# Optimization experiments

Hardware: AMD Instinct MI355X
Metric: run time of the kernel (lower is better)

## Reference

```python
import jax, jax.numpy as jnp
import numpy as np

B, T, D, H, DK = 4, 1024, 512, 8, 64
L = 2 * T - 1  # relative position length
EPS = 1e-3     # keras LayerNormalization default epsilon


def rel_shift(x, klen):
    # x: [B, H, T, L] with L = 2T-1 -> [B, H, T, klen] (Transformer-XL shift)
    b, h, t, l = x.shape
    x = x.reshape(b, h, l, t)[:, :, 1:, :]
    x = x.reshape(b, h, t, l - 1)
    return x[:, :, :, :klen]


def setup_inputs() -> dict:
    key = jax.random.key(0)
    ks = jax.random.split(key, 16)
    s = 0.02
    return {
        "x": jax.random.normal(ks[0], (B, T, D), jnp.float32),
        "pos": jax.random.normal(ks[1], (B, L, D), jnp.float32),
        "content_bias": jax.random.normal(ks[2], (H, DK), jnp.float32) * s,
        "pos_bias": jax.random.normal(ks[3], (H, DK), jnp.float32) * s,
        "gamma": jnp.ones((D,), jnp.float32),
        "beta": jnp.zeros((D,), jnp.float32),
        "Wq": jax.random.normal(ks[4], (D, H, DK), jnp.float32) * s,
        "bq": jnp.zeros((H, DK), jnp.float32),
        "Wk": jax.random.normal(ks[5], (D, H, DK), jnp.float32) * s,
        "bk": jnp.zeros((H, DK), jnp.float32),
        "Wv": jax.random.normal(ks[6], (D, H, DK), jnp.float32) * s,
        "bv": jnp.zeros((H, DK), jnp.float32),
        "Wp": jax.random.normal(ks[7], (D, H, DK), jnp.float32) * s,
        "Wo": jax.random.normal(ks[8], (H, DK, D), jnp.float32) * s,
        "bo": jnp.zeros((D,), jnp.float32),
    }


def reference(x, pos, content_bias, pos_bias, gamma, beta,
              Wq, bq, Wk, bk, Wv, bv, Wp, Wo, bo):
    # pre-norm LayerNorm
    mean = jnp.mean(x, axis=-1, keepdims=True)
    var = jnp.var(x, axis=-1, keepdims=True)
    y = (x - mean) * jax.lax.rsqrt(var + EPS) * gamma + beta

    # per-head projections
    q = jnp.einsum("bid,dhk->bihk", y, Wq) + bq      # [B,T,H,DK]
    k = jnp.einsum("bjd,dhk->bjhk", y, Wk) + bk
    v = jnp.einsum("bjd,dhk->bjhk", y, Wv) + bv
    p = jnp.einsum("bld,dhk->blhk", pos, Wp)          # [B,L,H,DK], no bias

    # Transformer-XL content + positional scores
    content = jnp.einsum("bihk,bjhk->bhij", q + content_bias, k)   # [B,H,T,T]
    positional = jnp.einsum("bihk,blhk->bhil", q + pos_bias, p)    # [B,H,T,L]
    positional = rel_shift(positional, content.shape[-1])          # [B,H,T,T]

    scores = (content + positional) / np.sqrt(DK).astype(np.float32)
    attn = jax.nn.softmax(scores, axis=-1)

    o = jnp.einsum("bhij,bjhk->bihk", attn, v)       # [B,T,H,DK]
    out = jnp.einsum("bihk,hkd->bid", o, Wo) + bo    # [B,T,D]

    # dropout is identity at inference; residual with factor=1.0
    return x + out
```

## Files before the change

kernel.cpp:

```cpp
#include <hip/hip_runtime.h>
#include <hip/hip_bf16.h>

typedef __hip_bfloat16 bf16;
typedef __attribute__((ext_vector_type(8))) short short8;
typedef __attribute__((ext_vector_type(4))) float f32x4;

#define B_  4
#define T_  1024
#define D_  512
#define H_  8
#define DK_ 64
#define L_  2047

__device__ __forceinline__ float b2f(bf16 v) { return __bfloat162float(v); }
__device__ __forceinline__ bf16  f2b(float v) { return __float2bfloat16(v); }
__device__ __forceinline__ float bits2f(unsigned short u) {
    return __uint_as_float(((unsigned int)u) << 16);
}
__device__ __forceinline__ unsigned short fbits(float v) {
    bf16 h = f2b(v); return *(unsigned short*)&h;
}

#define MFMA16(a, b, c) __builtin_amdgcn_mfma_f32_16x16x32_bf16(a, b, c, 0, 0, 0)
#define GLD_LDS16(g, l) __builtin_amdgcn_global_load_lds( \
    (const __attribute__((address_space(1))) unsigned int*)(g), \
    (__attribute__((address_space(3))) unsigned int*)(l), 16, 0, 0)

__global__ __launch_bounds__(256) void prep_all(
        const float* __restrict__ Wq, const float* __restrict__ Wk,
        const float* __restrict__ Wv, const float* __restrict__ Wp,
        const float* __restrict__ Wo,
        const float* __restrict__ bq, const float* __restrict__ bk,
        const float* __restrict__ bv,
        const float* __restrict__ pos, const float* __restrict__ x,
        const float* __restrict__ gamma, const float* __restrict__ beta,
        bf16* __restrict__ Wqkv_t, bf16* __restrict__ Wp_t, bf16* __restrict__ Wo_t,
        float* __restrict__ biasq, bf16* __restrict__ pos_bf, bf16* __restrict__ y) {
    __shared__ float tl[32][33];
    __shared__ float ws1[4], ws2[4];
    const int blk = blockIdx.x;
    const int t = threadIdx.x;

    if (blk < 1280) {
        const int z = blk >> 8, rem = blk & 255;
        const float* W; bf16* Wt; int roff;
        switch (z) {
            case 0: W = Wq; Wt = Wqkv_t; roff = 0;    break;
            case 1: W = Wk; Wt = Wqkv_t; roff = 512;  break;
            case 2: W = Wv; Wt = Wqkv_t; roff = 1024; break;
            case 3: W = Wp; Wt = Wp_t;   roff = 0;    break;
            default: W = Wo; Wt = Wo_t;  roff = 0;    break;
        }
        const int n0 = (rem & 15) * 32, k0 = (rem >> 4) * 32;
        const int tx = t & 31, ty = t >> 5;
#pragma unroll
        for (int r = 0; r < 4; ++r)
            tl[ty + r * 8][tx] = W[(size_t)(k0 + ty + r * 8) * 512 + n0 + tx];
        __syncthreads();
#pragma unroll
        for (int r = 0; r < 4; ++r)
            Wt[(size_t)(roff + n0 + ty + r * 8) * 512 + k0 + tx] = f2b(tl[tx][ty + r * 8]);
    } else if (blk < 1286) {
        int i = (blk - 1280) * 256 + t;
        biasq[i] = (i < 512) ? bq[i] : (i < 1024) ? bk[i - 512] : bv[i - 1024];
    } else if (blk < 3333) {
        size_t i = ((size_t)(blk - 1286) * 256 + t) * 8;
        float4 a = *(const float4*)(pos + i);
        float4 c = *(const float4*)(pos + i + 4);
        uint4 wv;
        wv.x = ((unsigned)fbits(a.y) << 16) | fbits(a.x);
        wv.y = ((unsigned)fbits(a.w) << 16) | fbits(a.z);
        wv.z = ((unsigned)fbits(c.y) << 16) | fbits(c.x);
        wv.w = ((unsigned)fbits(c.w) << 16) | fbits(c.z);
        *(uint4*)((unsigned short*)pos_bf + i) = wv;
    } else {
        const int row = blk - 3333;
        const float* xr = x + (size_t)row * D_;
        float v0 = xr[t];
        float v1 = xr[t + 256];
        float s  = v0 + v1;
        float s2 = v0 * v0 + v1 * v1;
#pragma unroll
        for (int off = 32; off > 0; off >>= 1) {
            s  += __shfl_down(s,  off, 64);
            s2 += __shfl_down(s2, off, 64);
        }
        const int wid = t >> 6, lane = t & 63;
        if (!lane) { ws1[wid] = s; ws2[wid] = s2; }
        __syncthreads();
        float S  = ws1[0] + ws1[1] + ws1[2] + ws1[3];
        float S2 = ws2[0] + ws2[1] + ws2[2] + ws2[3];
        float mean = S * (1.f / D_);
        float var  = S2 * (1.f / D_) - mean * mean;
        float r = rsqrtf(var + 1e-3f);
        bf16* yr = y + (size_t)row * D_;
        yr[t]       = f2b((v0 - mean) * r * gamma[t]       + beta[t]);
        yr[t + 256] = f2b((v1 - mean) * r * gamma[t + 256] + beta[t + 256]);
    }
}

template <bool C_F32>
__device__ __forceinline__ void gemm_body(
        const bf16* __restrict__ A, const bf16* __restrict__ Wt,
        const float* __restrict__ bias, const float* __restrict__ resid,
        void* __restrict__ Cv, int M, size_t seg_elems, int m0, int n0,
        unsigned short (*A_s)[32], unsigned short (*B_s)[32]) {
    const int t = threadIdx.x;
    const int w = t >> 6, lane = t & 63;
    const int quad = lane >> 4, n16 = lane & 15;
    const int wm = (w >> 1) * 64, wn = (w & 1) * 64;

    f32x4 acc[4][4];
#pragma unroll
    for (int a = 0; a < 4; ++a)
#pragma unroll
        for (int b = 0; b < 4; ++b) acc[a][b] = (f32x4){0.f, 0.f, 0.f, 0.f};

    const int ar = lane >> 2, ac8 = (lane & 3) * 8;
    auto stage = [&](int k0, int buf) {
        const int bo = buf << 7;
#pragma unroll
        for (int ps = 0; ps < 2; ++ps) {
            int br = (ps * 4 + w) * 16;
            GLD_LDS16(A  + (size_t)(m0 + br + ar) * 512 + k0 + ac8, &A_s[bo + br][0]);
            GLD_LDS16(Wt + (size_t)(n0 + br + ar) * 512 + k0 + ac8, &B_s[bo + br][0]);
        }
    };
    stage(0, 0);
    int cur = 0;
    for (int k0 = 0; k0 < 512; k0 += 32) {
        __syncthreads();
        if (k0 + 32 < 512) stage(k0 + 32, cur ^ 1);
        const int bo = cur << 7;
        short8 af[4], bfr[4];
#pragma unroll
        for (int i = 0; i < 4; ++i) {
            af[i]  = *(const short8*)&A_s[bo + wm + i * 16 + n16][quad * 8];
            bfr[i] = *(const short8*)&B_s[bo + wn + i * 16 + n16][quad * 8];
        }
#pragma unroll
        for (int mi = 0; mi < 4; ++mi)
#pragma unroll
            for (int ni = 0; ni < 4; ++ni)
                acc[mi][ni] = MFMA16(af[mi], bfr[ni], acc[mi][ni]);
        cur ^= 1;
    }

    const int seg = n0 >> 9;
#pragma unroll
    for (int mi = 0; mi < 4; ++mi) {
#pragma unroll
        for (int r = 0; r < 4; ++r) {
            int row = m0 + wm + mi * 16 + quad * 4 + r;
            if (row >= M) continue;
#pragma unroll
            for (int ni = 0; ni < 4; ++ni) {
                int col  = n0 + wn + ni * 16 + n16;
                int coll = col & 511;
                float vv = acc[mi][ni][r];
                if (bias) vv += bias[col];
                if constexpr (C_F32) {
                    float* C = (float*)Cv + seg * seg_elems;
                    if (resid) vv += resid[(size_t)row * 512 + coll];
                    C[(size_t)row * 512 + coll] = vv;
                } else {
                    bf16* C = (bf16*)Cv + seg * seg_elems;
                    C[(size_t)row * 512 + coll] = f2b(vv);
                }
            }
        }
    }
}

__global__ __launch_bounds__(256) void gemm_qkvp(
        const bf16* __restrict__ y, const bf16* __restrict__ pos_bf,
        const bf16* __restrict__ Wqkv_t, const bf16* __restrict__ Wp_t,
        const float* __restrict__ biasq,
        bf16* __restrict__ q, bf16* __restrict__ p, size_t seg_elems) {
    __shared__ __align__(16) unsigned short A_s[256][32];
    __shared__ __align__(16) unsigned short B_s[256][32];
    const int gid = blockIdx.x;
    if (gid < 384) {
        const int xcd = gid & 7, s = gid >> 3;
        const int n = s % 12;
        const int m = xcd * 4 + s / 12;
        gemm_body<false>(y, Wqkv_t, biasq, nullptr, q, 4096, seg_elems,
                         m * 128, n * 128, A_s, B_s);
    } else {
        const int g2 = gid - 384;
        const int xcd = g2 & 7, s = g2 >> 3;
        const int n = s & 3;
        const int m = xcd * 8 + (s >> 2);
        gemm_body<false>(pos_bf, Wp_t, nullptr, nullptr, p, 8188, 0,
                         m * 128, n * 128, A_s, B_s);
    }
}

__global__ __launch_bounds__(256) void gemm_out(
        const bf16* __restrict__ o, const bf16* __restrict__ Wo_t,
        const float* __restrict__ bo, const float* __restrict__ x,
        float* __restrict__ out) {
    __shared__ __align__(16) unsigned short A_s[256][32];
    __shared__ __align__(16) unsigned short B_s[256][32];
    const int xcd = blockIdx.x & 7, s = blockIdx.x >> 3;
    const int n = s & 3;
    const int m = xcd * 4 + (s >> 2);
    gemm_body<true>(o, Wo_t, bo, x, out, 4096, 0, m * 128, n * 128, A_s, B_s);
}

__global__ __launch_bounds__(256) void attn_mfma_kernel(
        const bf16* __restrict__ q, const bf16* __restrict__ k,
        const bf16* __restrict__ v, const bf16* __restrict__ p,
        const float* __restrict__ cbias, const float* __restrict__ pbias,
        bf16* __restrict__ o) {
    __shared__ __align__(16) unsigned short k_s[2][4096];
    __shared__ __align__(16) unsigned short pw_s[2][8192];
    __shared__ __align__(16) unsigned short vt_s[2][64][72];
    __shared__ __align__(16) unsigned short gbuf[4][16][72];
    __shared__ float cb_s[64], pb_s[64];
    __shared__ float wrap_s;

    const int fid  = blockIdx.x;
    const int xcd  = fid & 7;
    const int slot = fid >> 3;
    const int i0   = (slot & 15) * 64;
    const int g    = (slot >> 4) * 8 + xcd;
    const int h    = g & 7;
    const int b    = g >> 3;

    const int t  = threadIdx.x;
    const int w    = t >> 6;
    const int lane = t & 63;
    const int quad = lane >> 4;
    const int n16  = lane & 15;
    const int h64  = h * 64;
    const float sc_scale = 0.125f * 1.4426950408889634f;

    if (t < 64)       cb_s[t]      = cbias[h64 + t];
    else if (t < 128) pb_s[t - 64] = pbias[h64 + t - 64];

    const int l8 = lane >> 3, l7 = lane & 7;
    const int clog8 = (l7 ^ l8) * 8;
    const unsigned short* ksrc[2];
    const unsigned short* psrc[4];
#pragma unroll
    for (int ps = 0; ps < 2; ++ps) {
        int row = (w * 2 + ps) * 8 + l8;
        ksrc[ps] = (const unsigned short*)k + ((size_t)(b * T_ + row) * 512 + h64 + clog8);
    }
    const int slb = T_ - i0 - 63;
#pragma unroll
    for (int ps = 0; ps < 4; ++ps) {
        int row = (w * 4 + ps) * 8 + l8;
        psrc[ps] = (const unsigned short*)p + ((size_t)(b * L_ + slb + row) * 512 + h64 + clog8);
    }
    auto stage = [&](int j0n, int nxt) {
        size_t joff = (size_t)j0n * 512;
#pragma unroll
        for (int ps = 0; ps < 2; ++ps)
            GLD_LDS16(ksrc[ps] + joff, &k_s[nxt][(w * 2 + ps) * 512]);
#pragma unroll
        for (int ps = 0; ps < 4; ++ps)
            GLD_LDS16(psrc[ps] + joff, &pw_s[nxt][(w * 4 + ps) * 512]);
    };

    const int vd2 = (t & 31) * 2, vjg = t >> 5;
    const unsigned short* vsrc = (const unsigned short*)v +
        ((size_t)(b * T_ + vjg * 8) * 512 + h64 + vd2);
    unsigned int vReg[8];
    auto vload = [&](int j0n) {
        const unsigned short* vg = vsrc + (size_t)j0n * 512;
#pragma unroll
        for (int e = 0; e < 8; ++e) vReg[e] = *(const unsigned int*)(vg + (size_t)e * 512);
    };
    auto vwrite = [&](int nxt) {
        uint4 wlo, whi;
        wlo.x = (vReg[0] & 0xffffu) | (vReg[1] << 16);
        wlo.y = (vReg[2] & 0xffffu) | (vReg[3] << 16);
        wlo.z = (vReg[4] & 0xffffu) | (vReg[5] << 16);
        wlo.w = (vReg[6] & 0xffffu) | (vReg[7] << 16);
        whi.x = (vReg[0] >> 16) | (vReg[1] & 0xffff0000u);
        whi.y = (vReg[2] >> 16) | (vReg[3] & 0xffff0000u);
        whi.z = (vReg[4] >> 16) | (vReg[5] & 0xffff0000u);
        whi.w = (vReg[6] >> 16) | (vReg[7] & 0xffff0000u);
        *(uint4*)&vt_s[nxt][vd2][vjg * 8]     = wlo;
        *(uint4*)&vt_s[nxt][vd2 + 1][vjg * 8] = whi;
    };

    stage(0, 0);
    vload(0);
    __syncthreads();

    short8 ac[2], ap[2];
    {
        const unsigned short* qrow = (const unsigned short*)q +
            ((size_t)(b * T_ + i0 + 16 * w + n16) * 512 + h64);
#pragma unroll
        for (int kc = 0; kc < 2; ++kc) {
            uint4 u = *(const uint4*)(qrow + kc * 32 + quad * 8);
            const unsigned short* uv = (const unsigned short*)&u;
            unsigned short* acp = (unsigned short*)&ac[kc];
            unsigned short* app = (unsigned short*)&ap[kc];
#pragma unroll
            for (int e = 0; e < 8; ++e) {
                int d = kc * 32 + quad * 8 + e;
                float qv = bits2f(uv[e]);
                acp[e] = fbits((qv + cb_s[d]) * sc_scale);
                app[e] = fbits((qv + pb_s[d]) * sc_scale);
            }
        }
    }
    if (i0 == 0 && t < 64) {
        float part = (b2f(q[(size_t)(b * T_ + 1) * 512 + h64 + t]) + pb_s[t]) *
                     b2f(p[(size_t)(b * L_) * 512 + h64 + t]);
#pragma unroll
        for (int m = 1; m < 64; m <<= 1) part += __shfl_xor(part, m, 64);
        if (t == 0) wrap_s = part * sc_scale;
    }
    vwrite(0);

    int srcl[4]; bool hi[4];
#pragma unroll
    for (int r = 0; r < 4; ++r) {
        int ii = quad * 4 + r;
        srcl[r] = (lane & 48) | ((n16 - ii - 1) & 15);
        hi[r]   = n16 > ii;
    }
    short8 onesb;
    {
        const short ov = (n16 == 0) ? (short)0x3F80 : (short)0;
#pragma unroll
        for (int e = 0; e < 8; ++e) onesb[e] = ov;
    }

    const int pwoff = 48 - 16 * w;
    const int swzA  = (quad ^ (n16 & 7)) * 16;
    const int swzB  = swzA ^ 64;

    f32x4 O[4], O4;
#pragma unroll
    for (int nt = 0; nt < 4; ++nt) O[nt] = (f32x4){0.f, 0.f, 0.f, 0.f};
    O4 = (f32x4){0.f, 0.f, 0.f, 0.f};

    int cur = 0;
    for (int j0 = 0; j0 < T_; j0 += 64) {
        __syncthreads();
        const int nxt = cur ^ 1;
        const bool pre = (j0 + 64 < T_);
        if (pre) { vload(j0 + 64); stage(j0 + 64, nxt); }

        const char* krA  = (const char*)&k_s[cur][0]  + n16 * 128 + swzA;
        const char* krB  = krA + (swzB - swzA);
        const char* pwrA = (const char*)&pw_s[cur][0] + (pwoff + n16) * 128 + swzA;
        const char* pwrB = pwrA + (swzB - swzA);

        f32x4 Sc[4], G[5];
#pragma unroll
        for (int nt = 0; nt < 4; ++nt) Sc[nt] = (f32x4){0.f, 0.f, 0.f, 0.f};
#pragma unroll
        for (int ct = 0; ct < 5; ++ct) G[ct] = (f32x4){0.f, 0.f, 0.f, 0.f};
        __builtin_amdgcn_s_setprio(1);
#pragma unroll
        for (int kc = 0; kc < 2; ++kc) {
#pragma unroll
            for (int nt = 0; nt < 4; ++nt) {
                short8 bk = *(const short8*)((kc ? krB : krA) + nt * 2048);
                Sc[nt] = MFMA16(ac[kc], bk, Sc[nt]);
            }
#pragma unroll
            for (int ct = 0; ct < 5; ++ct) {
                short8 bp = *(const short8*)((kc ? pwrB : pwrA) + ct * 2048);
                G[ct] = MFMA16(ap[kc], bp, G[ct]);
            }
        }
        __builtin_amdgcn_s_setprio(0);

        float pe[4][4];
#pragma unroll
        for (int r = 0; r < 4; ++r) {
            float s0 = __shfl(G[0][r], srcl[r], 64);
            float s1 = __shfl(G[1][r], srcl[r], 64);
            float s2 = __shfl(G[2][r], srcl[r], 64);
            float s3 = __shfl(G[3][r], srcl[r], 64);
            float s4 = __shfl(G[4][r], srcl[r], 64);
            pe[0][r] = Sc[0][r] + (hi[r] ? s1 : s0);
            pe[1][r] = Sc[1][r] + (hi[r] ? s2 : s1);
            pe[2][r] = Sc[2][r] + (hi[r] ? s3 : s2);
            pe[3][r] = Sc[3][r] + (hi[r] ? s4 : s3);
        }
        if (i0 == 0 && w == 0 && j0 == 960 && lane == 15)
            pe[3][0] = Sc[3][0] + wrap_s;
#pragma unroll
        for (int ct = 0; ct < 4; ++ct)
#pragma unroll
            for (int r = 0; r < 4; ++r)
                *(bf16*)&gbuf[w][quad * 4 + r][ct * 16 + n16] = f2b(exp2f(pe[ct][r]));

        __builtin_amdgcn_s_setprio(1);
#pragma unroll
        for (int kc = 0; kc < 2; ++kc) {
            short8 pa = *(const short8*)&gbuf[w][n16][kc * 32 + quad * 8];
#pragma unroll
            for (int nt = 0; nt < 4; ++nt) {
                short8 vb = *(const short8*)&vt_s[cur][nt * 16 + n16][kc * 32 + quad * 8];
                O[nt] = MFMA16(pa, vb, O[nt]);
            }
            O4 = MFMA16(pa, onesb, O4);
        }
        __builtin_amdgcn_s_setprio(0);

        if (pre) vwrite(nxt);
        cur = nxt;
    }

#pragma unroll
    for (int r = 0; r < 4; ++r) {
        float l = __shfl(O4[r], lane & 48, 64);
        float inv = 1.f / l;
        int row = i0 + 16 * w + quad * 4 + r;
#pragma unroll
        for (int nt = 0; nt < 4; ++nt)
            o[(size_t)(b * T_ + row) * 512 + h64 + nt * 16 + n16] = f2b(O[nt][r] * inv);
    }
}

extern "C" void kernel_launch(void* const* d_in, const int* in_sizes, int n_in,
                              void* d_out, int out_size, void* d_ws, size_t ws_size,
                              hipStream_t stream) {
    (void)in_sizes; (void)n_in; (void)out_size;
    const float* x     = (const float*)d_in[0];
    const float* pos   = (const float*)d_in[1];
    const float* cb    = (const float*)d_in[2];
    const float* pb    = (const float*)d_in[3];
    const float* gamma = (const float*)d_in[4];
    const float* beta  = (const float*)d_in[5];
    const float* Wq    = (const float*)d_in[6];
    const float* bq    = (const float*)d_in[7];
    const float* Wk    = (const float*)d_in[8];
    const float* bk    = (const float*)d_in[9];
    const float* Wv    = (const float*)d_in[10];
    const float* bv    = (const float*)d_in[11];
    const float* Wp    = (const float*)d_in[12];
    const float* Wo    = (const float*)d_in[13];
    const float* bo    = (const float*)d_in[14];
    float* out = (float*)d_out;

    const int BT = B_ * T_;

    const size_t sz_bt = (size_t)BT * D_;
    const size_t sz_bl = (size_t)(B_ * L_) * D_;
    const size_t sz_w  = 512 * 512;
    const size_t need  = (5 * sz_bt + sz_bl + 5 * sz_w) * sizeof(bf16) + 1536 * sizeof(float);
    if (ws_size < need) return;

    bf16* y       = (bf16*)d_ws;
    bf16* o       = y + sz_bt;
    bf16* q       = y + 2 * sz_bt;
    bf16* k       = y + 3 * sz_bt;
    bf16* v       = y + 4 * sz_bt;
    bf16* p       = y + 5 * sz_bt;
    bf16* Wqkv_t  = p + sz_bl;
    bf16* Wp_t    = Wqkv_t + 3 * sz_w;
    bf16* Wo_t    = Wp_t + sz_w;
    float* biasq  = (float*)(Wo_t + sz_w);
    bf16* pos_bf  = (bf16*)d_out;

    prep_all<<<7429, 256, 0, stream>>>(Wq, Wk, Wv, Wp, Wo, bq, bk, bv, pos, x,
                                       gamma, beta, Wqkv_t, Wp_t, Wo_t, biasq, pos_bf, y);

    gemm_qkvp<<<640, 256, 0, stream>>>(y, pos_bf, Wqkv_t, Wp_t, biasq, q, p, sz_bt);

    attn_mfma_kernel<<<512, 256, 0, stream>>>(q, k, v, p, cb, pb, o);

    gemm_out<<<128, 256, 0, stream>>>(o, Wo_t, bo, x, out);
}
```

Before: 209.1 us.

## Software-pipeline attention loop: overlap next tile QK with current softmax-PV

```diff
diff --git a/kernel.cpp b/kernel.cpp
--- a/kernel.cpp
+++ b/kernel.cpp
@@ -208,7 +208,7 @@
     gemm_body<true>(o, Wo_t, bo, x, out, 4096, 0, m * 128, n * 128, A_s, B_s);
 }
 
-__global__ __launch_bounds__(256) void attn_mfma_kernel(
+__global__ __launch_bounds__(256, 2) void attn_mfma_kernel(
         const bf16* __restrict__ q, const bf16* __restrict__ k,
         const bf16* __restrict__ v, const bf16* __restrict__ p,
         const float* __restrict__ cbias, const float* __restrict__ pbias,
@@ -220,14 +220,9 @@
     __shared__ float cb_s[64], pb_s[64];
     __shared__ float wrap_s;
 
-    const int fid  = blockIdx.x;
-    const int xcd  = fid & 7;
-    const int slot = fid >> 3;
-    const int i0   = (slot & 15) * 64;
-    const int g    = (slot >> 4) * 8 + xcd;
-    const int h    = g & 7;
-    const int b    = g >> 3;
-
+    const int i0 = blockIdx.x * 64;
+    const int h  = blockIdx.y;
+    const int b  = blockIdx.z;
     const int t  = threadIdx.x;
     const int w    = t >> 6;
     const int lane = t & 63;
@@ -317,14 +312,13 @@
         for (int m = 1; m < 64; m <<= 1) part += __shfl_xor(part, m, 64);
         if (t == 0) wrap_s = part * sc_scale;
     }
-    vwrite(0);
-
-    int srcl[4]; bool hi[4];
+
+    int srcl[4]; bool hi_[4];
 #pragma unroll
     for (int r = 0; r < 4; ++r) {
         int ii = quad * 4 + r;
         srcl[r] = (lane & 48) | ((n16 - ii - 1) & 15);
-        hi[r]   = n16 > ii;
+        hi_[r]  = n16 > ii;
     }
     short8 onesb;
     {
@@ -342,24 +336,15 @@
     for (int nt = 0; nt < 4; ++nt) O[nt] = (f32x4){0.f, 0.f, 0.f, 0.f};
     O4 = (f32x4){0.f, 0.f, 0.f, 0.f};
 
-    int cur = 0;
-    for (int j0 = 0; j0 < T_; j0 += 64) {
-        __syncthreads();
-        const int nxt = cur ^ 1;
-        const bool pre = (j0 + 64 < T_);
-        if (pre) { vload(j0 + 64); stage(j0 + 64, nxt); }
-
-        const char* krA  = (const char*)&k_s[cur][0]  + n16 * 128 + swzA;
-        const char* krB  = krA + (swzB - swzA);
-        const char* pwrA = (const char*)&pw_s[cur][0] + (pwoff + n16) * 128 + swzA;
-        const char* pwrB = pwrA + (swzB - swzA);
-
-        f32x4 Sc[4], G[5];
+    auto qk = [&](f32x4 (&Sc)[4], f32x4 (&G)[5], int buf) {
+        const char* krA  = (const char*)&k_s[buf][0]  + n16 * 128 + swzA;
+        const char* krB  = (const char*)&k_s[buf][0]  + n16 * 128 + swzB;
+        const char* pwrA = (const char*)&pw_s[buf][0] + (pwoff + n16) * 128 + swzA;
+        const char* pwrB = (const char*)&pw_s[buf][0] + (pwoff + n16) * 128 + swzB;
 #pragma unroll
         for (int nt = 0; nt < 4; ++nt) Sc[nt] = (f32x4){0.f, 0.f, 0.f, 0.f};
 #pragma unroll
         for (int ct = 0; ct < 5; ++ct) G[ct] = (f32x4){0.f, 0.f, 0.f, 0.f};
-        __builtin_amdgcn_s_setprio(1);
 #pragma unroll
         for (int kc = 0; kc < 2; ++kc) {
 #pragma unroll
@@ -373,8 +358,9 @@
                 G[ct] = MFMA16(ap[kc], bp, G[ct]);
             }
         }
-        __builtin_amdgcn_s_setprio(0);
-
+    };
+
+    auto sm_pv = [&](const f32x4 (&Sc)[4], const f32x4 (&G)[5], int vb, bool dowrap) {
         float pe[4][4];
 #pragma unroll
         for (int r = 0; r < 4; ++r) {
@@ -383,35 +369,55 @@
             float s2 = __shfl(G[2][r], srcl[r], 64);
             float s3 = __shfl(G[3][r], srcl[r], 64);
             float s4 = __shfl(G[4][r], srcl[r], 64);
-            pe[0][r] = Sc[0][r] + (hi[r] ? s1 : s0);
-            pe[1][r] = Sc[1][r] + (hi[r] ? s2 : s1);
-            pe[2][r] = Sc[2][r] + (hi[r] ? s3 : s2);
-            pe[3][r] = Sc[3][r] + (hi[r] ? s4 : s3);
-        }
-        if (i0 == 0 && w == 0 && j0 == 960 && lane == 15)
+            pe[0][r] = Sc[0][r] + (hi_[r] ? s1 : s0);
+            pe[1][r] = Sc[1][r] + (hi_[r] ? s2 : s1);
+            pe[2][r] = Sc[2][r] + (hi_[r] ? s3 : s2);
+            pe[3][r] = Sc[3][r] + (hi_[r] ? s4 : s3);
+        }
+        if (dowrap && i0 == 0 && w == 0 && lane == 15)
             pe[3][0] = Sc[3][0] + wrap_s;
 #pragma unroll
         for (int ct = 0; ct < 4; ++ct)
 #pragma unroll
             for (int r = 0; r < 4; ++r)
                 *(bf16*)&gbuf[w][quad * 4 + r][ct * 16 + n16] = f2b(exp2f(pe[ct][r]));
-
-        __builtin_amdgcn_s_setprio(1);
 #pragma unroll
         for (int kc = 0; kc < 2; ++kc) {
             short8 pa = *(const short8*)&gbuf[w][n16][kc * 32 + quad * 8];
 #pragma unroll
             for (int nt = 0; nt < 4; ++nt) {
-                short8 vb = *(const short8*)&vt_s[cur][nt * 16 + n16][kc * 32 + quad * 8];
-                O[nt] = MFMA16(pa, vb, O[nt]);
+                short8 vb8 = *(const short8*)&vt_s[vb][nt * 16 + n16][kc * 32 + quad * 8];
+                O[nt] = MFMA16(pa, vb8, O[nt]);
             }
             O4 = MFMA16(pa, onesb, O4);
         }
-        __builtin_amdgcn_s_setprio(0);
-
-        if (pre) vwrite(nxt);
-        cur = nxt;
-    }
+    };
+
+    f32x4 ScA[4], GA[5], ScB[4], GB[5];
+
+    vwrite(0);
+    stage(64, 1);
+    vload(64);
+    qk(ScA, GA, 0);
+
+    auto body = [&](int tt, f32x4 (&ScC)[4], f32x4 (&GC)[5],
+                    const f32x4 (&ScP)[4], const f32x4 (&GP)[5], bool more) {
+        __syncthreads();
+        vwrite(tt & 1);
+        if (more) { stage((tt + 1) * 64, (tt + 1) & 1); vload((tt + 1) * 64); }
+        qk(ScC, GC, tt & 1);
+        sm_pv(ScP, GP, (tt - 1) & 1, false);
+    };
+
+#pragma unroll
+    for (int tp = 0; tp < 7; ++tp) {
+        body(2 * tp + 1, ScB, GB, ScA, GA, true);
+        body(2 * tp + 2, ScA, GA, ScB, GB, true);
+    }
+    body(15, ScB, GB, ScA, GA, false);
+
+    __syncthreads();
+    sm_pv(ScB, GB, 1, true);
 
 #pragma unroll
     for (int r = 0; r < 4; ++r) {
@@ -470,7 +476,7 @@
 
     gemm_qkvp<<<640, 256, 0, stream>>>(y, pos_bf, Wqkv_t, Wp_t, biasq, q, p, sz_bt);
 
-    attn_mfma_kernel<<<512, 256, 0, stream>>>(q, k, v, p, cb, pb, o);
+    attn_mfma_kernel<<<dim3(T_ / 64, H_, B_), 256, 0, stream>>>(q, k, v, p, cb, pb, o);
 
     gemm_out<<<128, 256, 0, stream>>>(o, Wo_t, bo, x, out);
 }
```

After: 208.4 us. Within noise of the previous version (-0.3%).
